# Kernel tuning notes

Measured on AMD Instinct MI355X. Metric: run time of the kernel, lower is better.

Reference implementation:

```python
import jax, jax.numpy as jnp
import numpy as np

B, N, D, R, H, E = 4, 8192, 16, 32, 64, 262144


def _linear_init(key, fan_in, fan_out):
    return jax.random.normal(key, (fan_in, fan_out), jnp.float32) * (1.0 / np.sqrt(fan_in))


def setup_inputs() -> dict:
    key = jax.random.key(0)
    ks = jax.random.split(key, 8)
    particles = jax.random.normal(ks[0], (B, N, D), jnp.float32)
    senders = jax.random.randint(ks[1], (E,), 0, N, dtype=jnp.int32)
    receivers = jax.random.randint(ks[2], (E,), 0, N, dtype=jnp.int32)
    # relation_encoder: Linear(2D->H), ReLU, Linear(H->R), ReLU
    W1 = _linear_init(ks[3], 2 * D, H)
    b1 = jnp.zeros((H,), jnp.float32)
    W2 = _linear_init(ks[4], H, R)
    b2 = jnp.zeros((R,), jnp.float32)
    # dynamics_fn: Linear(D+R->H), ReLU, Linear(H->D)
    W3 = _linear_init(ks[5], D + R, H)
    b3 = jnp.zeros((H,), jnp.float32)
    W4 = _linear_init(ks[6], H, D)
    b4 = jnp.zeros((D,), jnp.float32)
    return {"particles": particles, "senders": senders, "receivers": receivers,
            "W1": W1, "b1": b1, "W2": W2, "b2": b2,
            "W3": W3, "b3": b3, "W4": W4, "b4": b4}


def reference(particles, senders, receivers, W1, b1, W2, b2, W3, b3, W4, b4):
    # Gather per-edge sender/receiver states: [B, E, D]
    send = particles[:, senders, :]
    recv = particles[:, receivers, :]
    edge_in = jnp.concatenate([send, recv], axis=-1)          # [B, E, 2D]
    # relation_encoder (one batched GEMM over all edges)
    h = jax.nn.relu(edge_in @ W1 + b1)                        # [B, E, H]
    rel_feat = jax.nn.relu(h @ W2 + b2)                       # [B, E, R]
    # scatter-add edge features into receiver nodes
    Bp, Np, _ = particles.shape
    rel = jnp.zeros((Bp, Np, rel_feat.shape[-1]), particles.dtype)
    rel = rel.at[:, receivers, :].add(rel_feat)               # [B, N, R]
    # node update MLP
    dyn_in = jnp.concatenate([particles, rel], axis=-1)       # [B, N, D+R]
    delta = jax.nn.relu(dyn_in @ W3 + b3) @ W4 + b4           # [B, N, D]
    return particles + delta
```

## Files before the change

### kernel.cpp

```cpp
#include <hip/hip_runtime.h>
#include <hip/hip_bf16.h>

namespace {

constexpr int B = 4;
constexpr int N = 8192;
constexpr int D = 16;
constexpr int R = 32;
constexpr int H = 64;
constexpr int E = 262144;

typedef __attribute__((ext_vector_type(8))) short short8;
typedef __attribute__((ext_vector_type(4))) short short4v;
typedef __attribute__((ext_vector_type(4))) float f32x4;

__device__ __forceinline__ float4 ld4(const float* p) {
    return *reinterpret_cast<const float4*>(p);
}
__device__ __forceinline__ float4 fma4(float a, float4 w, float4 c) {
    return float4{fmaf(a, w.x, c.x), fmaf(a, w.y, c.y),
                  fmaf(a, w.z, c.z), fmaf(a, w.w, c.w)};
}
__device__ __forceinline__ float4 relu4(float4 v) {
    return float4{fmaxf(v.x, 0.f), fmaxf(v.y, 0.f), fmaxf(v.z, 0.f), fmaxf(v.w, 0.f)};
}
__device__ __forceinline__ short bf16s(float f) {
    __hip_bfloat16 h = __float2bfloat16(f);
    return __builtin_bit_cast(short, h);
}
__device__ __forceinline__ short8 pack8(float4 a, float4 b) {
    short8 o;
    o[0] = bf16s(a.x); o[1] = bf16s(a.y); o[2] = bf16s(a.z); o[3] = bf16s(a.w);
    o[4] = bf16s(b.x); o[5] = bf16s(b.y); o[6] = bf16s(b.z); o[7] = bf16s(b.w);
    return o;
}
__device__ __forceinline__ short4v pack4_relu(f32x4 c) {
    short4v o;
    o[0] = bf16s(fmaxf(c[0], 0.f)); o[1] = bf16s(fmaxf(c[1], 0.f));
    o[2] = bf16s(fmaxf(c[2], 0.f)); o[3] = bf16s(fmaxf(c[3], 0.f));
    return o;
}
__device__ __forceinline__ short8 cat44(short4v a, short4v b) {
    int2 ia = __builtin_bit_cast(int2, a);
    int2 ib = __builtin_bit_cast(int2, b);
    int4 v{ia.x, ia.y, ib.x, ib.y};
    return __builtin_bit_cast(short8, v);
}
__device__ __forceinline__ float red_get(const int4* uu, int i) {
    const int wsel = i >> 1;
    const int4 v = uu[wsel >> 2];
    const int word = (wsel & 3) == 0 ? v.x : (wsel & 3) == 1 ? v.y
                   : (wsel & 3) == 2 ? v.z : v.w;
    return (i & 1) ? __builtin_bit_cast(float, word & 0xffff0000)
                   : __builtin_bit_cast(float, (unsigned)word << 16);
}

constexpr int RED_S = 264;


__device__ __forceinline__ void prepack_w12(
    int t, const float* __restrict__ W1, const float* __restrict__ W2,
    short* __restrict__ w1p, short* __restrict__ w2p)
{
    for (int i = t; i < 4 * 64 * 8; i += 256) {
        int j = i & 7, lane = (i >> 3) & 63, ct = i >> 9;
        int k = (lane >> 4) * 8 + j, n = ct * 16 + (lane & 15);
        w1p[i] = bf16s(W1[k * H + n]);
    }
    for (int i = t; i < 4 * 64 * 8; i += 256) {
        int j = i & 7, lane = (i >> 3) & 63, idx = i >> 9;
        int ct = idx >> 1, kc = idx & 1;
        int k = kc * 32 + (j >> 2) * 16 + ((lane >> 4) & 3) * 4 + (j & 3);
        int f = ct * 16 + (lane & 15);
        w2p[i] = bf16s(W2[k * R + f]);
    }
}
__device__ __forceinline__ void prepack_w34(
    int t, const float* __restrict__ W3, const float* __restrict__ W4,
    short* __restrict__ w3p, short* __restrict__ w4p)
{
    for (int i = t; i < 8 * 64 * 8; i += 256) {
        int j = i & 7, lane = (i >> 3) & 63, idx = i >> 9;
        int ct = idx >> 1, kc = idx & 1;
        int k = kc * 32 + (lane >> 4) * 8 + j, n = ct * 16 + (lane & 15);
        w3p[i] = (k < D + R) ? bf16s(W3[k * H + n]) : (short)0;
    }
    for (int i = t; i < 2 * 64 * 8; i += 256) {
        int j = i & 7, lane = (i >> 3) & 63, kc = i >> 9;
        int k = kc * 32 + (j >> 2) * 16 + ((lane >> 4) & 3) * 4 + (j & 3);
        int d = lane & 15;
        w4p[i] = bf16s(W4[k * D + d]);
    }
}

__global__ __launch_bounds__(256) void histscan_prepack_kernel(
    const int* __restrict__ receivers, int* __restrict__ cnt,
    int* __restrict__ done, int* __restrict__ pos,
    const float* __restrict__ W1, const float* __restrict__ W2,
    const float* __restrict__ W3, const float* __restrict__ W4,
    short* __restrict__ w1p, short* __restrict__ w2p,
    short* __restrict__ w3p, short* __restrict__ w4p,
    float4* __restrict__ relz)
{
    const int tid = threadIdx.x;

    if (blockIdx.x >= 1024) {
        if (blockIdx.x == 1024) {
            prepack_w12(tid, W1, W2, w1p, w2p);
            prepack_w34(tid, W3, W4, w3p, w4p);
        } else {
            const int base = (blockIdx.x - 1025) * 256 + tid;
            #pragma unroll
            for (int i = 0; i < 8; ++i)
                relz[base + i * 32768] = float4{0.f, 0.f, 0.f, 0.f};
        }
        return;
    }

    atomicAdd(cnt + receivers[blockIdx.x * 256 + tid], 1);
    __syncthreads();

    __shared__ int amlast;
    if (tid == 0) {
        const int old = atomicAdd(done, 1);
        amlast = (old == 1023) ? 1 : 0;
    }
    __syncthreads();
    if (!amlast) return;

    int c[32];
    int s = 0;
    const int cb = tid * 32;
    #pragma unroll
    for (int i = 0; i < 32; ++i) {
        c[i] = __hip_atomic_load(cnt + cb + i, __ATOMIC_RELAXED,
                                 __HIP_MEMORY_SCOPE_AGENT);
        s += c[i];
    }
    const int lane = tid & 63;
    const int wv   = tid >> 6;
    int incl = s;
    #pragma unroll
    for (int d = 1; d < 64; d <<= 1) {
        int v = __shfl_up(incl, d, 64);
        if (lane >= d) incl += v;
    }
    __shared__ int wtot[4];
    if (lane == 63) wtot[wv] = incl;
    __syncthreads();
    int base = incl - s;
    #pragma unroll
    for (int i = 0; i < 4; ++i) base += (i < wv) ? wtot[i] : 0;
    #pragma unroll
    for (int i = 0; i < 32; ++i) {
        pos[cb + i] = base;
        base += c[i];
    }
}

__global__ __launch_bounds__(256) void scatter_kernel(
    const int* __restrict__ senders, const int* __restrict__ receivers,
    int* __restrict__ pos, int2* __restrict__ sr)
{
    int e = blockIdx.x * 256 + threadIdx.x;
    if (e < E) {
        int r = receivers[e];
        int p = atomicAdd(pos + r, 1);
        sr[p] = int2{senders[e], r};
    }
}

__global__ __launch_bounds__(256, 4) void edge_mfma_kernel(
    const float* __restrict__ particles,
    const int2*  __restrict__ sr,
    const short* __restrict__ w1p, const float* __restrict__ b1,
    const short* __restrict__ w2p, const float* __restrict__ b2,
    float* __restrict__ rel)
{
    __shared__ short red[R * RED_S];
    __shared__ int   rs[256];
    __shared__ float pre[8][33];
    __shared__ float suf[8][33];
    __shared__ int   kcnt[8];

    const int tid  = threadIdx.x;
    const int lane = tid & 63;
    const int w    = tid >> 6;
    const int b    = blockIdx.x >> 10;
    const int p0   = (blockIdx.x & 1023) * 256;
    const int l15  = lane & 15;
    const int q    = lane >> 4;

    const int2 srv = sr[p0 + tid];
    rs[tid] = srv.y;

    float4 a0[4], a1[4];
    #pragma unroll
    for (int t = 0; t < 4; ++t) {
        int srow = __shfl(srv.x, t * 16 + l15);
        int rrow = __shfl(srv.y, t * 16 + l15);
        int row = (q < 2) ? srow : rrow;
        const float* src = particles + ((size_t)b * N + row) * D + (q & 1) * 8;
        a0[t] = ld4(src);
        a1[t] = ld4(src + 4);
    }

    short8 w1f[4], w2f[4];
    #pragma unroll
    for (int mt = 0; mt < 4; ++mt)
        w1f[mt] = *reinterpret_cast<const short8*>(w1p + (mt * 64 + lane) * 8);
    #pragma unroll
    for (int i = 0; i < 4; ++i)
        w2f[i] = *reinterpret_cast<const short8*>(w2p + (i * 64 + lane) * 8);

    f32x4 bias1[4];
    #pragma unroll
    for (int mt = 0; mt < 4; ++mt) {
        float4 t4 = ld4(b1 + mt * 16 + q * 4);
        bias1[mt] = f32x4{t4.x, t4.y, t4.z, t4.w};
    }
    const float bias2a = b2[l15];
    const float bias2b = b2[16 + l15];

    short8 af[4];
    #pragma unroll
    for (int t = 0; t < 4; ++t) af[t] = pack8(a0[t], a1[t]);

    #pragma unroll
    for (int t = 0; t < 4; ++t) {
        f32x4 c0 = __builtin_amdgcn_mfma_f32_16x16x32_bf16(w1f[0], af[t], bias1[0], 0, 0, 0);
        f32x4 c1 = __builtin_amdgcn_mfma_f32_16x16x32_bf16(w1f[1], af[t], bias1[1], 0, 0, 0);
        f32x4 c2 = __builtin_amdgcn_mfma_f32_16x16x32_bf16(w1f[2], af[t], bias1[2], 0, 0, 0);
        f32x4 c3 = __builtin_amdgcn_mfma_f32_16x16x32_bf16(w1f[3], af[t], bias1[3], 0, 0, 0);
        short8 h0 = cat44(pack4_relu(c0), pack4_relu(c1));
        short8 h1 = cat44(pack4_relu(c2), pack4_relu(c3));

        f32x4 r0 = {bias2a, bias2a, bias2a, bias2a};
        f32x4 r1 = {bias2b, bias2b, bias2b, bias2b};
        r0 = __builtin_amdgcn_mfma_f32_16x16x32_bf16(h0, w2f[0], r0, 0, 0, 0);
        r0 = __builtin_amdgcn_mfma_f32_16x16x32_bf16(h1, w2f[1], r0, 0, 0, 0);
        r1 = __builtin_amdgcn_mfma_f32_16x16x32_bf16(h0, w2f[2], r1, 0, 0, 0);
        r1 = __builtin_amdgcn_mfma_f32_16x16x32_bf16(h1, w2f[3], r1, 0, 0, 0);

        const int pb2 = w * 64 + t * 16 + q * 4;
        *reinterpret_cast<short4v*>(red + l15 * RED_S + pb2)        = pack4_relu(r0);
        *reinterpret_cast<short4v*>(red + (16 + l15) * RED_S + pb2) = pack4_relu(r1);
    }
    __syncthreads();

    const int g2 = tid >> 5;
    const int f  = tid & 31;
    const int gb = g2 * 32;
    float* relb = rel + (size_t)b * N * R;

    unsigned bmask = 0;
    int first;
    {
        int4 r4[8];
        #pragma unroll
        for (int i = 0; i < 8; ++i)
            r4[i] = *reinterpret_cast<const int4*>(rs + gb + 4 * i);
        first = r4[0].x;
        int prev = first;
        #pragma unroll
        for (int i = 1; i < 32; ++i) {
            const int4 v4 = r4[i >> 2];
            const int rr = (i & 3) == 0 ? v4.x : (i & 3) == 1 ? v4.y
                         : (i & 3) == 2 ? v4.z : v4.w;
            if (rr != prev) bmask |= (1u << i);
            prev = rr;
        }
    }
    if (f == 0) kcnt[g2] = __popc(bmask) + 1;

    int4 uu[4];
    #pragma unroll
    for (int i = 0; i < 4; ++i)
        uu[i] = *reinterpret_cast<const int4*>(red + f * RED_S + gb + 8 * i);

    {
        float acc = 0.f;
        int cur = first;
        int seg = 0;
        #pragma unroll
        for (int i = 0; i < 32; ++i) {
            if (bmask & (1u << i)) {
                if (seg == 0) pre[g2][f] = acc;
                else relb[(size_t)cur * R + f] = acc;
                ++seg;
                acc = 0.f;
                cur = rs[gb + i];
            }
            acc += red_get(uu, i);
        }
        suf[g2][f] = acc;
    }
    __syncthreads();

    if (tid < 32) {
        int   cur2 = rs[0];
        float a2   = 0.f;
        int   nfl  = 0;
        #pragma unroll
        for (int g = 0; g < 8; ++g) {
            const int   rf   = rs[g * 32];
            const int   rl   = rs[g * 32 + 31];
            const int   kk   = kcnt[g];
            const float sufv = suf[g][tid];
            if (kk == 1) {
                if (rf == cur2) a2 += sufv;
                else {
                    if (nfl == 0) atomicAdd(relb + (size_t)cur2 * R + tid, a2);
                    else          relb[(size_t)cur2 * R + tid] = a2;
                    ++nfl;
                    cur2 = rf; a2 = sufv;
                }
            } else {
                const float prev = pre[g][tid];
                if (rf == cur2) {
                    a2 += prev;
                    if (nfl == 0) atomicAdd(relb + (size_t)cur2 * R + tid, a2);
                    else          relb[(size_t)cur2 * R + tid] = a2;
                    ++nfl;
                } else {
                    if (nfl == 0) atomicAdd(relb + (size_t)cur2 * R + tid, a2);
                    else          relb[(size_t)cur2 * R + tid] = a2;
                    ++nfl;
                    relb[(size_t)rf * R + tid] = prev;
                    ++nfl;
                }
                cur2 = rl; a2 = sufv;
            }
        }
        atomicAdd(relb + (size_t)cur2 * R + tid, a2);
    }
}

__global__ __launch_bounds__(256, 4) void node_mfma_kernel(
    const float* __restrict__ particles,
    const float* __restrict__ rel,
    const short* __restrict__ w3p, const float* __restrict__ b3,
    const short* __restrict__ w4p, const float* __restrict__ b4,
    float* __restrict__ out)
{
    const int tid  = threadIdx.x;
    const int lane = tid & 63;
    const int w    = tid >> 6;
    const int tile = blockIdx.x * 4 + w;
    const int b    = tile >> 9;
    const int l15  = lane & 15;
    const int q    = lane >> 4;
    const int node = (tile & 511) * 16 + l15;

    const float* prow = particles + ((size_t)b * N + node) * D;
    const float* rrow = rel + ((size_t)b * N + node) * R;

    const float* src0 = (q < 2) ? (prow + (q & 1) * 8) : (rrow + (q & 1) * 8);
    float4 c0a = ld4(src0), c0b = ld4(src0 + 4);
    float4 c1a = {0.f, 0.f, 0.f, 0.f}, c1b = {0.f, 0.f, 0.f, 0.f};
    if (q < 2) { c1a = ld4(rrow + 16 + q * 8); c1b = ld4(rrow + 20 + q * 8); }

    short8 w3f[8], w4f[2];
    #pragma unroll
    for (int i = 0; i < 8; ++i)
        w3f[i] = *reinterpret_cast<const short8*>(w3p + (i * 64 + lane) * 8);
    #pragma unroll
    for (int i = 0; i < 2; ++i)
        w4f[i] = *reinterpret_cast<const short8*>(w4p + (i * 64 + lane) * 8);

    f32x4 bias3[4];
    #pragma unroll
    for (int mt = 0; mt < 4; ++mt) {
        float4 t4 = ld4(b3 + mt * 16 + q * 4);
        bias3[mt] = f32x4{t4.x, t4.y, t4.z, t4.w};
    }
    f32x4 bias4;
    { float4 t4 = ld4(b4 + q * 4); bias4 = f32x4{t4.x, t4.y, t4.z, t4.w}; }

    short8 a0 = pack8(c0a, c0b);
    short8 a1 = pack8(c1a, c1b);

    f32x4 c0 = bias3[0], c1 = bias3[1], c2 = bias3[2], c3 = bias3[3];
    c0 = __builtin_amdgcn_mfma_f32_16x16x32_bf16(w3f[0], a0, c0, 0, 0, 0);
    c0 = __builtin_amdgcn_mfma_f32_16x16x32_bf16(w3f[1], a1, c0, 0, 0, 0);
    c1 = __builtin_amdgcn_mfma_f32_16x16x32_bf16(w3f[2], a0, c1, 0, 0, 0);
    c1 = __builtin_amdgcn_mfma_f32_16x16x32_bf16(w3f[3], a1, c1, 0, 0, 0);
    c2 = __builtin_amdgcn_mfma_f32_16x16x32_bf16(w3f[4], a0, c2, 0, 0, 0);
    c2 = __builtin_amdgcn_mfma_f32_16x16x32_bf16(w3f[5], a1, c2, 0, 0, 0);
    c3 = __builtin_amdgcn_mfma_f32_16x16x32_bf16(w3f[6], a0, c3, 0, 0, 0);
    c3 = __builtin_amdgcn_mfma_f32_16x16x32_bf16(w3f[7], a1, c3, 0, 0, 0);
    short8 h0 = cat44(pack4_relu(c0), pack4_relu(c1));
    short8 h1 = cat44(pack4_relu(c2), pack4_relu(c3));

    f32x4 r = bias4;
    r = __builtin_amdgcn_mfma_f32_16x16x32_bf16(w4f[0], h0, r, 0, 0, 0);
    r = __builtin_amdgcn_mfma_f32_16x16x32_bf16(w4f[1], h1, r, 0, 0, 0);

    float4 pv = ld4(prow + q * 4);
    float4* po = reinterpret_cast<float4*>(out + ((size_t)b * N + node) * D + q * 4);
    *po = float4{pv.x + r[0], pv.y + r[1], pv.z + r[2], pv.w + r[3]};
}


__global__ __launch_bounds__(256, 2) void edge_atomic_kernel(
    const float* __restrict__ particles,
    const int*   __restrict__ senders,
    const int*   __restrict__ receivers,
    const float* __restrict__ W1, const float* __restrict__ b1,
    const float* __restrict__ W2, const float* __restrict__ b2,
    float* __restrict__ rel)
{
    const int idx = blockIdx.x * 256 + threadIdx.x;
    const int b = idx >> 18;
    const int e = idx & (E - 1);
    const int s = senders[e];
    const int r = receivers[e];

    float4 ein4[8];
    {
        const float4* ps = reinterpret_cast<const float4*>(particles + ((size_t)b * N + s) * D);
        const float4* pr = reinterpret_cast<const float4*>(particles + ((size_t)b * N + r) * D);
        #pragma unroll
        for (int qq = 0; qq < 4; ++qq) ein4[qq] = ps[qq];
        #pragma unroll
        for (int qq = 0; qq < 4; ++qq) ein4[4 + qq] = pr[qq];
    }
    float4 rf4[8];
    #pragma unroll
    for (int qq = 0; qq < 8; ++qq) rf4[qq] = ld4(b2 + 4 * qq);

    for (int j4 = 0; j4 < H / 4; ++j4) {
        float4 h = ld4(b1 + 4 * j4);
        const float* w1c = W1 + 4 * j4;
        #pragma unroll
        for (int kv = 0; kv < 8; ++kv) {
            const float4 ev = ein4[kv];
            h = fma4(ev.x, ld4(w1c + (4 * kv + 0) * H), h);
            h = fma4(ev.y, ld4(w1c + (4 * kv + 1) * H), h);
            h = fma4(ev.z, ld4(w1c + (4 * kv + 2) * H), h);
            h = fma4(ev.w, ld4(w1c + (4 * kv + 3) * H), h);
        }
        h = relu4(h);
        const float* w2r = W2 + (4 * j4) * R;
        #pragma unroll
        for (int qq = 0; qq < 4; ++qq) {
            const float hq = (qq == 0) ? h.x : (qq == 1) ? h.y : (qq == 2) ? h.z : h.w;
            #pragma unroll
            for (int r4 = 0; r4 < 8; ++r4)
                rf4[r4] = fma4(hq, ld4(w2r + qq * R + 4 * r4), rf4[r4]);
        }
    }
    float* dst = rel + ((size_t)b * N + r) * R;
    #pragma unroll
    for (int r4 = 0; r4 < 8; ++r4) {
        float4 v = relu4(rf4[r4]);
        atomicAdd(dst + 4 * r4 + 0, v.x);
        atomicAdd(dst + 4 * r4 + 1, v.y);
        atomicAdd(dst + 4 * r4 + 2, v.z);
        atomicAdd(dst + 4 * r4 + 3, v.w);
    }
}

__global__ __launch_bounds__(256, 2) void node_valu_kernel(
    const float* __restrict__ particles,
    const float* __restrict__ rel,
    const float* __restrict__ W3, const float* __restrict__ b3,
    const float* __restrict__ W4, const float* __restrict__ b4,
    float* __restrict__ out)
{
    const int idx = blockIdx.x * 256 + threadIdx.x;
    float4 in4[12];
    {
        const float4* pp = reinterpret_cast<const float4*>(particles + (size_t)idx * D);
        #pragma unroll
        for (int qq = 0; qq < 4; ++qq) in4[qq] = pp[qq];
        const float4* pr = reinterpret_cast<const float4*>(rel + (size_t)idx * R);
        #pragma unroll
        for (int qq = 0; qq < 8; ++qq) in4[4 + qq] = pr[qq];
    }
    float4 dl4[4];
    #pragma unroll
    for (int qq = 0; qq < 4; ++qq) dl4[qq] = ld4(b4 + 4 * qq);

    for (int j4 = 0; j4 < H / 4; ++j4) {
        float4 h = ld4(b3 + 4 * j4);
        const float* w3c = W3 + 4 * j4;
        #pragma unroll
        for (int kv = 0; kv < 12; ++kv) {
            const float4 ev = in4[kv];
            h = fma4(ev.x, ld4(w3c + (4 * kv + 0) * H), h);
            h = fma4(ev.y, ld4(w3c + (4 * kv + 1) * H), h);
            h = fma4(ev.z, ld4(w3c + (4 * kv + 2) * H), h);
            h = fma4(ev.w, ld4(w3c + (4 * kv + 3) * H), h);
        }
        h = relu4(h);
        const float* w4r = W4 + (4 * j4) * D;
        #pragma unroll
        for (int qq = 0; qq < 4; ++qq) {
            const float hq = (qq == 0) ? h.x : (qq == 1) ? h.y : (qq == 2) ? h.z : h.w;
            #pragma unroll
            for (int d4 = 0; d4 < 4; ++d4)
                dl4[d4] = fma4(hq, ld4(w4r + qq * D + 4 * d4), dl4[d4]);
        }
    }
    float4* po = reinterpret_cast<float4*>(out + (size_t)idx * D);
    #pragma unroll
    for (int qq = 0; qq < 4; ++qq) {
        float4 v = dl4[qq];
        float4 pv = in4[qq];
        po[qq] = float4{pv.x + v.x, pv.y + v.y, pv.z + v.z, pv.w + v.w};
    }
}

}

extern "C" void kernel_launch(void* const* d_in, const int* in_sizes, int n_in,
                              void* d_out, int out_size, void* d_ws, size_t ws_size,
                              hipStream_t stream) {
    const float* particles = (const float*)d_in[0];
    const int*   senders   = (const int*)d_in[1];
    const int*   receivers = (const int*)d_in[2];
    const float* W1 = (const float*)d_in[3];
    const float* b1 = (const float*)d_in[4];
    const float* W2 = (const float*)d_in[5];
    const float* b2 = (const float*)d_in[6];
    const float* W3 = (const float*)d_in[7];
    const float* b3 = (const float*)d_in[8];
    const float* W4 = (const float*)d_in[9];
    const float* b4 = (const float*)d_in[10];
    float* out = (float*)d_out;

    char* ws = (char*)d_ws;
    size_t off = 0;
    auto take = [&](size_t bytes) -> char* {
        char* p = ws + off;
        off = (off + bytes + 255) & ~(size_t)255;
        return p;
    };
    int*   cnt     = (int*)  take((size_t)N * 4);
    int*   done    = (int*)  take(4);
    int*   pos     = (int*)  take((size_t)N * 4);
    int2*  sr      = (int2*) take((size_t)E * 8);
    float* rel     = (float*)take((size_t)B * N * R * 4);
    short* w1p     = (short*)take((size_t)4 * 64 * 8 * 2);
    short* w2p     = (short*)take((size_t)4 * 64 * 8 * 2);
    short* w3p     = (short*)take((size_t)8 * 64 * 8 * 2);
    short* w4p     = (short*)take((size_t)2 * 64 * 8 * 2);
    const bool fast = (off <= ws_size);

    if (fast) {
        hipMemsetAsync(cnt, 0, (size_t)N * 4 + 4, stream);
        histscan_prepack_kernel<<<1153, 256, 0, stream>>>(
            receivers, cnt, done, pos,
            W1, W2, W3, W4, w1p, w2p, w3p, w4p, (float4*)rel);
        scatter_kernel<<<E / 256, 256, 0, stream>>>(senders, receivers, pos, sr);
        edge_mfma_kernel<<<(B * E) / 256, 256, 0, stream>>>(
            particles, sr, w1p, b1, w2p, b2, rel);
        node_mfma_kernel<<<(B * N / 16) / 4, 256, 0, stream>>>(
            particles, rel, w3p, b3, w4p, b4, out);
    } else {
        float* rel0 = (float*)d_ws;
        hipMemsetAsync(rel0, 0, (size_t)B * N * R * 4, stream);
        edge_atomic_kernel<<<(B * E) / 256, 256, 0, stream>>>(
            particles, senders, receivers, W1, b1, W2, b2, rel0);
        node_valu_kernel<<<(B * N) / 256, 256, 0, stream>>>(
            particles, rel0, W3, b3, W4, b4, out);
    }
}
```

Before: 155.8 us.

## Fuse histogram, scan and scatter into one kernel with grid-wide spin barriers

Merges the histogram/scan kernel and the scatter kernel into a single launch. Block 0 waits for all histogram blocks to finish, then computes the prefix scan and raises a flag, while the other blocks spin on that flag before scattering edges. This removes one kernel launch and its boundary gap. It relies on all 1024 sorting blocks being co-resident (launch bounds raised to 5 blocks per CU); if they are not, the spin-waits could deadlock.

```diff
diff --git a/kernel.cpp b/kernel.cpp
--- a/kernel.cpp
+++ b/kernel.cpp
@@ -93,9 +93,10 @@
     }
 }
 
-__global__ __launch_bounds__(256) void histscan_prepack_kernel(
-    const int* __restrict__ receivers, int* __restrict__ cnt,
-    int* __restrict__ done, int* __restrict__ pos,
+__global__ __launch_bounds__(256, 5) void megasort_kernel(
+    const int* __restrict__ senders, const int* __restrict__ receivers,
+    int* __restrict__ cnt, int* __restrict__ done, int* __restrict__ sflag,
+    int* __restrict__ pos, int2* __restrict__ sr,
     const float* __restrict__ W1, const float* __restrict__ W2,
     const float* __restrict__ W3, const float* __restrict__ W4,
     short* __restrict__ w1p, short* __restrict__ w2p,
@@ -103,13 +104,14 @@
     float4* __restrict__ relz)
 {
     const int tid = threadIdx.x;
-
-    if (blockIdx.x >= 1024) {
-        if (blockIdx.x == 1024) {
+    const int bid = blockIdx.x;
+
+    if (bid >= 1024) {
+        if (bid == 1024) {
             prepack_w12(tid, W1, W2, w1p, w2p);
             prepack_w34(tid, W3, W4, w3p, w4p);
         } else {
-            const int base = (blockIdx.x - 1025) * 256 + tid;
+            const int base = (bid - 1025) * 256 + tid;
             #pragma unroll
             for (int i = 0; i < 8; ++i)
                 relz[base + i * 32768] = float4{0.f, 0.f, 0.f, 0.f};
@@ -117,57 +119,70 @@
         return;
     }
 
-    atomicAdd(cnt + receivers[blockIdx.x * 256 + tid], 1);
+    const int e = bid * 256 + tid;
+    const int r = receivers[e];
+    const int s = senders[e];
+    atomicAdd(cnt + r, 1);
     __syncthreads();
-
-    __shared__ int amlast;
-    if (tid == 0) {
-        const int old = atomicAdd(done, 1);
-        amlast = (old == 1023) ? 1 : 0;
-    }
-    __syncthreads();
-    if (!amlast) return;
-
-    int c[32];
-    int s = 0;
-    const int cb = tid * 32;
-    #pragma unroll
-    for (int i = 0; i < 32; ++i) {
-        c[i] = __hip_atomic_load(cnt + cb + i, __ATOMIC_RELAXED,
-                                 __HIP_MEMORY_SCOPE_AGENT);
-        s += c[i];
-    }
-    const int lane = tid & 63;
-    const int wv   = tid >> 6;
-    int incl = s;
-    #pragma unroll
-    for (int d = 1; d < 64; d <<= 1) {
-        int v = __shfl_up(incl, d, 64);
-        if (lane >= d) incl += v;
-    }
-    __shared__ int wtot[4];
-    if (lane == 63) wtot[wv] = incl;
-    __syncthreads();
-    int base = incl - s;
-    #pragma unroll
-    for (int i = 0; i < 4; ++i) base += (i < wv) ? wtot[i] : 0;
-    #pragma unroll
-    for (int i = 0; i < 32; ++i) {
-        pos[cb + i] = base;
-        base += c[i];
-    }
-}
-
-__global__ __launch_bounds__(256) void scatter_kernel(
-    const int* __restrict__ senders, const int* __restrict__ receivers,
-    int* __restrict__ pos, int2* __restrict__ sr)
-{
-    int e = blockIdx.x * 256 + threadIdx.x;
-    if (e < E) {
-        int r = receivers[e];
-        int p = atomicAdd(pos + r, 1);
-        sr[p] = int2{senders[e], r};
-    }
+    if (tid == 0)
+        __hip_atomic_fetch_add(done, 1, __ATOMIC_RELEASE,
+                               __HIP_MEMORY_SCOPE_AGENT);
+
+    if (bid == 0) {
+        if (tid == 0) {
+            while (__hip_atomic_load(done, __ATOMIC_RELAXED,
+                                     __HIP_MEMORY_SCOPE_AGENT) < 1024)
+                __builtin_amdgcn_s_sleep(8);
+        }
+        __syncthreads();
+        __threadfence();
+
+        int4 c4[8];
+        const int4* cp = reinterpret_cast<const int4*>(cnt) + tid * 8;
+        #pragma unroll
+        for (int i = 0; i < 8; ++i) c4[i] = cp[i];
+        int s0 = 0;
+        #pragma unroll
+        for (int i = 0; i < 8; ++i) s0 += c4[i].x + c4[i].y + c4[i].z + c4[i].w;
+        const int lane = tid & 63, wv = tid >> 6;
+        int incl = s0;
+        #pragma unroll
+        for (int d2 = 1; d2 < 64; d2 <<= 1) {
+            int v = __shfl_up(incl, d2, 64);
+            if (lane >= d2) incl += v;
+        }
+        __shared__ int wtot[4];
+        if (lane == 63) wtot[wv] = incl;
+        __syncthreads();
+        int base = incl - s0;
+        #pragma unroll
+        for (int i = 0; i < 4; ++i) base += (i < wv) ? wtot[i] : 0;
+        int4* po = reinterpret_cast<int4*>(pos) + tid * 8;
+        #pragma unroll
+        for (int i = 0; i < 8; ++i) {
+            int4 cv = c4[i], o;
+            o.x = base; base += cv.x;
+            o.y = base; base += cv.y;
+            o.z = base; base += cv.z;
+            o.w = base; base += cv.w;
+            po[i] = o;
+        }
+        __syncthreads();
+        __threadfence();
+        if (tid == 0)
+            __hip_atomic_store(sflag, 1, __ATOMIC_RELEASE,
+                               __HIP_MEMORY_SCOPE_AGENT);
+    } else {
+        if (tid == 0) {
+            while (__hip_atomic_load(sflag, __ATOMIC_RELAXED,
+                                     __HIP_MEMORY_SCOPE_AGENT) == 0)
+                __builtin_amdgcn_s_sleep(8);
+        }
+        __syncthreads();
+    }
+
+    const int p = atomicAdd(pos + r, 1);
+    sr[p] = int2{s, r};
 }
 
 __global__ __launch_bounds__(256, 4) void edge_mfma_kernel(
@@ -537,8 +552,9 @@
         off = (off + bytes + 255) & ~(size_t)255;
         return p;
     };
-    int*   cnt     = (int*)  take((size_t)N * 4);
-    int*   done    = (int*)  take(4);
+    int*   cnt     = (int*)  take((size_t)N * 4 + 8);
+    int*   done    = cnt + N;
+    int*   sflag   = cnt + N + 1;
     int*   pos     = (int*)  take((size_t)N * 4);
     int2*  sr      = (int2*) take((size_t)E * 8);
     float* rel     = (float*)take((size_t)B * N * R * 4);
@@ -549,11 +565,10 @@
     const bool fast = (off <= ws_size);
 
     if (fast) {
-        hipMemsetAsync(cnt, 0, (size_t)N * 4 + 4, stream);
-        histscan_prepack_kernel<<<1153, 256, 0, stream>>>(
-            receivers, cnt, done, pos,
+        hipMemsetAsync(cnt, 0, (size_t)N * 4 + 8, stream);
+        megasort_kernel<<<1153, 256, 0, stream>>>(
+            senders, receivers, cnt, done, sflag, pos, sr,
             W1, W2, W3, W4, w1p, w2p, w3p, w4p, (float4*)rel);
-        scatter_kernel<<<E / 256, 256, 0, stream>>>(senders, receivers, pos, sr);
         edge_mfma_kernel<<<(B * E) / 256, 256, 0, stream>>>(
             particles, sr, w1p, b1, w2p, b2, rel);
         node_mfma_kernel<<<(B * N / 16) / 4, 256, 0, stream>>>(
```

New measurement: 207.0 us. 1.33x slower.
